# Optimization experiments

Hardware: AMD Instinct MI355X
Metric: run time of the kernel (lower is better)

## Reference

```python
import jax, jax.numpy as jnp
import numpy as np

D_MODEL = 512
D_FFN = 1024
B, N = 8, 2048


def setup_inputs() -> dict:
    key = jax.random.key(0)
    k1, k2, k3, k4, k5, k6 = jax.random.split(key, 6)
    x = jax.random.normal(k1, (B, N, D_MODEL), dtype=jnp.float32)
    interaction_mask = jax.random.randint(k2, (B, N, N), 0, 2).astype(jnp.float32)
    s1 = 1.0 / np.sqrt(D_MODEL)
    s2 = 1.0 / np.sqrt(D_FFN)
    W1 = jax.random.uniform(k3, (D_MODEL, D_FFN), jnp.float32, -s1, s1)
    b1 = jax.random.uniform(k4, (D_FFN,), jnp.float32, -s1, s1)
    W2 = jax.random.uniform(k5, (D_FFN, 3 * D_MODEL), jnp.float32, -s2, s2)
    b2 = jax.random.uniform(k6, (3 * D_MODEL,), jnp.float32, -s2, s2)
    return {"x": x, "interaction_mask": interaction_mask,
            "W1": W1, "b1": b1, "W2": W2, "b2": b2}


def reference(x, interaction_mask, W1, b1, W2, b2):
    # 2-layer FFN: Linear -> ReLU -> Linear (identity)
    h = jax.nn.relu(x @ W1 + b1)           # [B, N, d_ffn]
    kqv = h @ W2 + b2                        # [B, N, 3*d_model]
    k, q, v = jnp.split(kqv, 3, axis=-1)     # each [B, N, d_model]
    scale = D_MODEL ** -0.5
    # softmax-free scaled dot-product
    attn = jnp.einsum("bqd,bkd->bqk", q, k) * scale  # [B, N, N]
    attn = attn * interaction_mask
    return jnp.einsum("bqk,bkd->bqd", attn, v)        # [B, N, d_model]
```

## Files before the change

kernel.cpp:

```cpp
#include <hip/hip_runtime.h>
#include <hip/hip_bf16.h>

typedef __attribute__((ext_vector_type(8))) short bf16x8;
typedef __attribute__((ext_vector_type(4))) float f32x4;

#define NB 8
#define NN 2048
#define DM 512
#define DF 1024

__device__ __forceinline__ ushort f2b(float f) {
  union { __hip_bfloat16 h; ushort u; } c;
  c.h = __float2bfloat16(f);
  return c.u;
}
__device__ __forceinline__ float b2f(ushort u) {
  union { ushort u; __hip_bfloat16 h; } c;
  c.u = u;
  return __bfloat162float(c.h);
}

typedef __attribute__((address_space(1))) const void gvoid_t;
typedef __attribute__((address_space(3))) void svoid_t;
__device__ __forceinline__ void gload16(const void* g, void* s) {
  __builtin_amdgcn_global_load_lds((gvoid_t*)g, (svoid_t*)s, 16, 0, 0);
}

__device__ __forceinline__ void gemm_core_128(
    const ushort* __restrict__ A, const ushort* __restrict__ B,
    int K, int brow, int bcol, f32x4 (&acc)[4][4], ushort* smem)
{
  const int tid = threadIdx.x;
  const int w = tid >> 6, l = tid & 63;
  const int sr = (w << 3) + (l >> 3);
  const int sc = (((l & 7) ^ (l >> 3)) << 3);
  const int fr = l & 15;
  const int arow = ((w >> 1) << 6) + fr;
  const int brw  = ((w & 1) << 6) + fr;
  char* base = (char*)smem;
  char* A0 = base;          char* B0 = base + 16384;
  char* A1 = base + 32768;  char* B1 = base + 49152;

#pragma unroll
  for (int m = 0; m < 4; m++)
#pragma unroll
    for (int n = 0; n < 4; n++)
      acc[m][n] = (f32x4){0.f, 0.f, 0.f, 0.f};

  const ushort* Ap = A + (long)(brow + sr) * K + sc;
  const ushort* Bp = B + (long)(bcol + sr) * K + sc;
  const int nkt = K >> 6;

  auto stage = [&](char* Ad, char* Bd, int kt) {
#pragma unroll
    for (int i = 0; i < 4; i++) {
      gload16(Ap + (long)i * 32 * K + kt * 64, Ad + i * 4096 + (w << 10));
      gload16(Bp + (long)i * 32 * K + kt * 64, Bd + i * 4096 + (w << 10));
    }
  };
  auto compute = [&](const char* As_, const char* Bs_) {
#pragma unroll
    for (int kk = 0; kk < 2; kk++) {
      const int cx = ((((kk << 2) + (l >> 4)) ^ (l & 7)) << 4);
      bf16x8 a[4], b[4];
#pragma unroll
      for (int m = 0; m < 4; m++)
        a[m] = *(const bf16x8*)(As_ + (arow + m * 16) * 128 + cx);
#pragma unroll
      for (int n = 0; n < 4; n++)
        b[n] = *(const bf16x8*)(Bs_ + (brw + n * 16) * 128 + cx);
#pragma unroll
      for (int m = 0; m < 4; m++)
#pragma unroll
        for (int n = 0; n < 4; n++)
          acc[m][n] = __builtin_amdgcn_mfma_f32_16x16x32_bf16(a[m], b[n], acc[m][n], 0, 0, 0);
    }
  };

  stage(A0, B0, 0);
  __syncthreads();
  for (int kt = 0; kt < nkt; kt += 2) {
    stage(A1, B1, kt + 1);
    compute(A0, B0);
    __syncthreads();
    if (kt + 2 < nkt) stage(A0, B0, kt + 2);
    compute(A1, B1);
    __syncthreads();
  }
}

__device__ __forceinline__ void gemm_core_128_sb(
    const ushort* __restrict__ A, const ushort* __restrict__ B,
    int K, int brow, int bcol, f32x4 (&acc)[4][4], ushort* smem)
{
  ushort* As = smem;
  ushort* Bs = smem + 128 * 64;
  const int tid = threadIdx.x;
  const int w = tid >> 6, l = tid & 63;
  const int sr = (w << 3) + (l >> 3);
  const int sc = (((l & 7) ^ (l >> 3)) << 3);
  char* AsB = (char*)As;
  char* BsB = (char*)Bs;
  const int fr = l & 15;
  const int arow = ((w >> 1) << 6) + fr;
  const int brw  = ((w & 1) << 6) + fr;

#pragma unroll
  for (int m = 0; m < 4; m++)
#pragma unroll
    for (int n = 0; n < 4; n++)
      acc[m][n] = (f32x4){0.f, 0.f, 0.f, 0.f};

  const ushort* Ap = A + (long)(brow + sr) * K + sc;
  const ushort* Bp = B + (long)(bcol + sr) * K + sc;
  const int nkt = K >> 6;
  for (int kt = 0; kt < nkt; ++kt) {
#pragma unroll
    for (int i = 0; i < 4; i++) {
      gload16(Ap + (long)i * 32 * K, AsB + i * 4096 + (w << 10));
      gload16(Bp + (long)i * 32 * K, BsB + i * 4096 + (w << 10));
    }
    Ap += 64; Bp += 64;
    __syncthreads();
#pragma unroll
    for (int kk = 0; kk < 2; kk++) {
      const int cx = ((((kk << 2) + (l >> 4)) ^ (l & 7)) << 4);
      bf16x8 a[4], b[4];
#pragma unroll
      for (int m = 0; m < 4; m++)
        a[m] = *(const bf16x8*)(AsB + (arow + m * 16) * 128 + cx);
#pragma unroll
      for (int n = 0; n < 4; n++)
        b[n] = *(const bf16x8*)(BsB + (brw + n * 16) * 128 + cx);
#pragma unroll
      for (int m = 0; m < 4; m++)
#pragma unroll
        for (int n = 0; n < 4; n++)
          acc[m][n] = __builtin_amdgcn_mfma_f32_16x16x32_bf16(a[m], b[n], acc[m][n], 0, 0, 0);
    }
    __syncthreads();
  }
}

__device__ __forceinline__ void acc_to_lds_bf16(f32x4 (&acc)[4][4], ushort* smem) {
  const int tid = threadIdx.x, w = tid >> 6, l = tid & 63;
  const int r0l = ((w >> 1) << 6) + ((l >> 4) << 2);
  const int c0l = ((w & 1) << 6) + (l & 15);
#pragma unroll
  for (int n = 0; n < 4; n++)
#pragma unroll
    for (int m = 0; m < 4; m++)
#pragma unroll
      for (int j = 0; j < 4; j++)
        smem[(r0l + m * 16 + j) * 128 + (c0l + n * 16)] = f2b(acc[m][n][j]);
}


__global__ __launch_bounds__(256) void k_cvt(const float* __restrict__ in,
                                             ushort* __restrict__ out) {
  const long i = ((long)blockIdx.x * 256 + threadIdx.x) << 2;
  const float4 v = *(const float4*)(in + i);
  ushort4 o;
  o.x = f2b(v.x); o.y = f2b(v.y); o.z = f2b(v.z); o.w = f2b(v.w);
  *(ushort4*)(out + i) = o;
}

__device__ __forceinline__ float ld2f(const float* p, long i) { return p[i]; }
__device__ __forceinline__ float ld2f(const __hip_bfloat16* p, long i) { return __bfloat162float(p[i]); }

template <typename TIN>
__global__ __launch_bounds__(256) void k_tr(const TIN* __restrict__ in, ushort* __restrict__ out,
                                            int R, int C, long inB, long outB) {
  __shared__ float t[32][33];
  const long b = blockIdx.z;
  const TIN* ip = in + b * inB;
  ushort* op = out + b * outB;
  const int c0 = blockIdx.x << 5, r0 = blockIdx.y << 5;
  const int tx = threadIdx.x & 31, ty = threadIdx.x >> 5;
#pragma unroll
  for (int j = 0; j < 32; j += 8)
    t[ty + j][tx] = ld2f(ip, (long)(r0 + ty + j) * C + (c0 + tx));
  __syncthreads();
#pragma unroll
  for (int j = 0; j < 32; j += 8)
    op[(long)(c0 + ty + j) * R + (r0 + tx)] = f2b(t[tx][ty + j]);
}

__global__ __launch_bounds__(256) void k_gemm1(const ushort* __restrict__ xb,
                                               const ushort* __restrict__ w1t,
                                               const float* __restrict__ b1,
                                               ushort* __restrict__ hb) {
  __shared__ ushort smem[128 * 256];
  f32x4 acc[4][4];
  const int brow = blockIdx.x << 7, bcol = blockIdx.y << 7;
  gemm_core_128(xb, w1t, DM, brow, bcol, acc, smem);
  const int tid = threadIdx.x, w = tid >> 6, l = tid & 63;
  const int c0l = ((w & 1) << 6) + (l & 15);
#pragma unroll
  for (int n = 0; n < 4; n++) {
    const float bias = b1[bcol + c0l + n * 16];
#pragma unroll
    for (int m = 0; m < 4; m++)
#pragma unroll
      for (int j = 0; j < 4; j++) {
        float v = acc[m][n][j] + bias;
        acc[m][n][j] = v > 0.f ? v : 0.f;
      }
  }
  acc_to_lds_bf16(acc, smem);
  __syncthreads();
  const int rb = tid >> 4, cb = tid & 15;
#pragma unroll
  for (int i = 0; i < 8; i++) {
    const int row = i * 16 + rb;
    bf16x8 s = *(const bf16x8*)(smem + row * 128 + cb * 8);
    *(bf16x8*)(hb + (long)(brow + row) * DF + bcol + cb * 8) = s;
  }
}

__global__ __launch_bounds__(256) void k_gemm2(const ushort* __restrict__ hb,
                                               const ushort* __restrict__ w2t,
                                               const float* __restrict__ b2,
                                               ushort* __restrict__ kb,
                                               ushort* __restrict__ qb,
                                               ushort* __restrict__ vb) {
  __shared__ ushort smem[128 * 256];
  f32x4 acc[4][4];
  const int brow = blockIdx.x << 7, bcol = blockIdx.y << 7;
  gemm_core_128(hb, w2t, DF, brow, bcol, acc, smem);
  const int seg = bcol >> 9;
  ushort* dst = (seg == 0) ? kb : ((seg == 1) ? qb : vb);
  const float sc = (seg == 1) ? 0.04419417382415922f : 1.0f;
  const int tid = threadIdx.x, w = tid >> 6, l = tid & 63;
  const int c0l = ((w & 1) << 6) + (l & 15);
#pragma unroll
  for (int n = 0; n < 4; n++) {
    const float bias = b2[bcol + c0l + n * 16];
#pragma unroll
    for (int m = 0; m < 4; m++)
#pragma unroll
      for (int j = 0; j < 4; j++)
        acc[m][n][j] = (acc[m][n][j] + bias) * sc;
  }
  acc_to_lds_bf16(acc, smem);
  __syncthreads();
  const int rb = tid >> 4, cb = tid & 15;
  const int clb = bcol - (seg << 9);
#pragma unroll
  for (int i = 0; i < 8; i++) {
    const int row = i * 16 + rb;
    bf16x8 s = *(const bf16x8*)(smem + row * 128 + cb * 8);
    *(bf16x8*)(dst + (long)(brow + row) * DM + clb + cb * 8) = s;
  }
}

__global__ __launch_bounds__(256) void k_qk(const ushort* __restrict__ qb,
                                            const ushort* __restrict__ kb,
                                            const float* __restrict__ mask,
                                            ushort* __restrict__ Sbuf) {
  __shared__ ushort smem[128 * 128];
  const int orig = blockIdx.x;
  const int swz = (orig & 7) * 256 + (orig >> 3);
  const int bx = swz & 15, by = (swz >> 4) & 15, batch = swz >> 8;
  const int brow = bx << 7, bcol = by << 7;
  const ushort* A = qb + (long)batch * NN * DM;
  const ushort* Bm = kb + (long)batch * NN * DM;
  const float* mk = mask + (long)batch * NN * NN;
  ushort* S = Sbuf + (long)batch * NN * NN;

  f32x4 acc[4][4];
  gemm_core_128_sb(A, Bm, DM, brow, bcol, acc, smem);
  acc_to_lds_bf16(acc, smem);
  __syncthreads();

  const int tid = threadIdx.x, rb = tid >> 4, cb = tid & 15;
  float4 mreg[8][2];
#pragma unroll
  for (int i = 0; i < 8; i++) {
    const long goff = (long)(brow + i * 16 + rb) * NN + bcol + cb * 8;
    mreg[i][0] = *(const float4*)(mk + goff);
    mreg[i][1] = *(const float4*)(mk + goff + 4);
  }
#pragma unroll
  for (int i = 0; i < 8; i++) {
    const int row = i * 16 + rb;
    const long goff = (long)(brow + row) * NN + bcol + cb * 8;
    bf16x8 s = *(const bf16x8*)(smem + row * 128 + cb * 8);
    bf16x8 o;
    o[0] = (short)f2b(b2f((ushort)s[0]) * mreg[i][0].x);
    o[1] = (short)f2b(b2f((ushort)s[1]) * mreg[i][0].y);
    o[2] = (short)f2b(b2f((ushort)s[2]) * mreg[i][0].z);
    o[3] = (short)f2b(b2f((ushort)s[3]) * mreg[i][0].w);
    o[4] = (short)f2b(b2f((ushort)s[4]) * mreg[i][1].x);
    o[5] = (short)f2b(b2f((ushort)s[5]) * mreg[i][1].y);
    o[6] = (short)f2b(b2f((ushort)s[6]) * mreg[i][1].z);
    o[7] = (short)f2b(b2f((ushort)s[7]) * mreg[i][1].w);
    *(bf16x8*)(S + goff) = o;
  }
}

__global__ __launch_bounds__(256) void k_pv(const ushort* __restrict__ Sbuf,
                                            const ushort* __restrict__ vtb,
                                            float* __restrict__ out) {
  __shared__ ushort smem[128 * 256];
  const int batch = blockIdx.z;
  const ushort* A = Sbuf + (long)batch * NN * NN;
  const ushort* Bm = vtb + (long)batch * DM * NN;
  float* op = out + (long)batch * NN * DM;
  f32x4 acc[4][4];
  const int brow = blockIdx.x << 7, bcol = blockIdx.y << 7;
  gemm_core_128(A, Bm, NN, brow, bcol, acc, smem);
  const int tid = threadIdx.x, w = tid >> 6, l = tid & 63;
  const int r0 = brow + ((w >> 1) << 6) + ((l >> 4) << 2);
  const int c0 = bcol + ((w & 1) << 6) + (l & 15);
#pragma unroll
  for (int n = 0; n < 4; n++) {
    const int c = c0 + n * 16;
#pragma unroll
    for (int m = 0; m < 4; m++) {
      const int r = r0 + m * 16;
#pragma unroll
      for (int j = 0; j < 4; j++)
        op[(long)(r + j) * DM + c] = acc[m][n][j];
    }
  }
}

extern "C" void kernel_launch(void* const* d_in, const int* in_sizes, int n_in,
                              void* d_out, int out_size, void* d_ws, size_t ws_size,
                              hipStream_t stream) {
  const float* x    = (const float*)d_in[0];
  const float* mask = (const float*)d_in[1];
  const float* W1   = (const float*)d_in[2];
  const float* b1   = (const float*)d_in[3];
  const float* W2   = (const float*)d_in[4];
  const float* b2   = (const float*)d_in[5];
  float* out = (float*)d_out;

  char* ws = (char*)d_ws;
  size_t off = 0;
  auto alloc = [&](size_t n) { char* p = ws + off; off += (n + 255) & ~(size_t)255; return p; };
  ushort* xb  = (ushort*)alloc((size_t)NB * NN * DM * 2);
  ushort* hb  = (ushort*)alloc((size_t)NB * NN * DF * 2);
  ushort* w1t = (ushort*)alloc((size_t)DF * DM * 2);
  ushort* w2t = (ushort*)alloc((size_t)3 * DM * DF * 2);
  ushort* kb  = (ushort*)alloc((size_t)NB * NN * DM * 2);
  ushort* qb  = (ushort*)alloc((size_t)NB * NN * DM * 2);
  ushort* vb  = (ushort*)alloc((size_t)NB * NN * DM * 2);
  ushort* vtb = (ushort*)alloc((size_t)NB * NN * DM * 2);
  ushort* Sbuf = (ushort*)alloc((size_t)NB * NN * NN * 2);

  k_cvt<<<dim3(8192), dim3(256), 0, stream>>>(x, xb);
  k_tr<float><<<dim3(DF / 32, DM / 32, 1), dim3(256), 0, stream>>>(W1, w1t, DM, DF, 0, 0);
  k_tr<float><<<dim3(3 * DM / 32, DF / 32, 1), dim3(256), 0, stream>>>(W2, w2t, DF, 3 * DM, 0, 0);
  k_gemm1<<<dim3(NB * NN / 128, DF / 128), dim3(256), 0, stream>>>(xb, w1t, b1, hb);
  k_gemm2<<<dim3(NB * NN / 128, 3 * DM / 128), dim3(256), 0, stream>>>(hb, w2t, b2, kb, qb, vb);
  k_tr<__hip_bfloat16><<<dim3(DM / 32, NN / 32, NB), dim3(256), 0, stream>>>(
      (const __hip_bfloat16*)vb, vtb, NN, DM, (long)NN * DM, (long)DM * NN);
  k_qk<<<dim3(2048), dim3(256), 0, stream>>>(qb, kb, mask, Sbuf);
  k_pv<<<dim3(NN / 128, DM / 128, NB), dim3(256), 0, stream>>>(Sbuf, vtb, out);
}
```

Measured before the change: 220.0 us.

## Fuse V transpose into gemm2 epilogue, coalesce PV stores, simplify QK grid

New measurement: 209.7 us. 4.7% less time.

```diff
diff --git a/kernel.cpp b/kernel.cpp
--- a/kernel.cpp
+++ b/kernel.cpp
@@ -165,25 +165,18 @@
   *(ushort4*)(out + i) = o;
 }
 
-__device__ __forceinline__ float ld2f(const float* p, long i) { return p[i]; }
-__device__ __forceinline__ float ld2f(const __hip_bfloat16* p, long i) { return __bfloat162float(p[i]); }
-
-template <typename TIN>
-__global__ __launch_bounds__(256) void k_tr(const TIN* __restrict__ in, ushort* __restrict__ out,
-                                            int R, int C, long inB, long outB) {
+__global__ __launch_bounds__(256) void k_trw(const float* __restrict__ in, ushort* __restrict__ out,
+                                             int R, int C) {
   __shared__ float t[32][33];
-  const long b = blockIdx.z;
-  const TIN* ip = in + b * inB;
-  ushort* op = out + b * outB;
   const int c0 = blockIdx.x << 5, r0 = blockIdx.y << 5;
   const int tx = threadIdx.x & 31, ty = threadIdx.x >> 5;
 #pragma unroll
   for (int j = 0; j < 32; j += 8)
-    t[ty + j][tx] = ld2f(ip, (long)(r0 + ty + j) * C + (c0 + tx));
+    t[ty + j][tx] = in[(long)(r0 + ty + j) * C + (c0 + tx)];
   __syncthreads();
 #pragma unroll
   for (int j = 0; j < 32; j += 8)
-    op[(long)(c0 + ty + j) * R + (r0 + tx)] = f2b(t[tx][ty + j]);
+    out[(long)(c0 + ty + j) * R + (r0 + tx)] = f2b(t[tx][ty + j]);
 }
 
 __global__ __launch_bounds__(256) void k_gemm1(const ushort* __restrict__ xb,
@@ -223,13 +216,12 @@
                                                const float* __restrict__ b2,
                                                ushort* __restrict__ kb,
                                                ushort* __restrict__ qb,
-                                               ushort* __restrict__ vb) {
+                                               ushort* __restrict__ vtb) {
   __shared__ ushort smem[128 * 256];
   f32x4 acc[4][4];
   const int brow = blockIdx.x << 7, bcol = blockIdx.y << 7;
   gemm_core_128(hb, w2t, DF, brow, bcol, acc, smem);
   const int seg = bcol >> 9;
-  ushort* dst = (seg == 0) ? kb : ((seg == 1) ? qb : vb);
   const float sc = (seg == 1) ? 0.04419417382415922f : 1.0f;
   const int tid = threadIdx.x, w = tid >> 6, l = tid & 63;
   const int c0l = ((w & 1) << 6) + (l & 15);
@@ -244,13 +236,30 @@
   }
   acc_to_lds_bf16(acc, smem);
   __syncthreads();
-  const int rb = tid >> 4, cb = tid & 15;
   const int clb = bcol - (seg << 9);
-#pragma unroll
-  for (int i = 0; i < 8; i++) {
-    const int row = i * 16 + rb;
-    bf16x8 s = *(const bf16x8*)(smem + row * 128 + cb * 8);
-    *(bf16x8*)(dst + (long)(brow + row) * DM + clb + cb * 8) = s;
+  if (seg < 2) {
+    ushort* dst = (seg == 0) ? kb : qb;
+    const int rb = tid >> 4, cb = tid & 15;
+#pragma unroll
+    for (int i = 0; i < 8; i++) {
+      const int row = i * 16 + rb;
+      bf16x8 s = *(const bf16x8*)(smem + row * 128 + cb * 8);
+      *(bf16x8*)(dst + (long)(brow + row) * DM + clb + cb * 8) = s;
+    }
+  } else {
+    const int batch = brow >> 11;
+    const int rbase = brow & 2047;
+    const int c = tid & 127, rc = tid >> 7;
+    ushort* vt = vtb + (long)batch * DM * NN + (long)(clb + c) * NN + rbase;
+#pragma unroll
+    for (int it = 0; it < 8; ++it) {
+      const int chunk = rc * 8 + it;
+      bf16x8 o;
+#pragma unroll
+      for (int j = 0; j < 8; ++j)
+        o[j] = (short)smem[(chunk * 8 + j) * 128 + c];
+      *(bf16x8*)(vt + chunk * 8) = o;
+    }
   }
 }
 
@@ -259,42 +268,33 @@
                                             const float* __restrict__ mask,
                                             ushort* __restrict__ Sbuf) {
   __shared__ ushort smem[128 * 128];
-  const int orig = blockIdx.x;
-  const int swz = (orig & 7) * 256 + (orig >> 3);
-  const int bx = swz & 15, by = (swz >> 4) & 15, batch = swz >> 8;
-  const int brow = bx << 7, bcol = by << 7;
+  const int batch = blockIdx.z;
   const ushort* A = qb + (long)batch * NN * DM;
   const ushort* Bm = kb + (long)batch * NN * DM;
   const float* mk = mask + (long)batch * NN * NN;
   ushort* S = Sbuf + (long)batch * NN * NN;
-
   f32x4 acc[4][4];
+  const int brow = blockIdx.x << 7, bcol = blockIdx.y << 7;
   gemm_core_128_sb(A, Bm, DM, brow, bcol, acc, smem);
   acc_to_lds_bf16(acc, smem);
   __syncthreads();
-
   const int tid = threadIdx.x, rb = tid >> 4, cb = tid & 15;
-  float4 mreg[8][2];
-#pragma unroll
-  for (int i = 0; i < 8; i++) {
-    const long goff = (long)(brow + i * 16 + rb) * NN + bcol + cb * 8;
-    mreg[i][0] = *(const float4*)(mk + goff);
-    mreg[i][1] = *(const float4*)(mk + goff + 4);
-  }
 #pragma unroll
   for (int i = 0; i < 8; i++) {
     const int row = i * 16 + rb;
     const long goff = (long)(brow + row) * NN + bcol + cb * 8;
     bf16x8 s = *(const bf16x8*)(smem + row * 128 + cb * 8);
+    const float4 m0 = *(const float4*)(mk + goff);
+    const float4 m1 = *(const float4*)(mk + goff + 4);
     bf16x8 o;
-    o[0] = (short)f2b(b2f((ushort)s[0]) * mreg[i][0].x);
-    o[1] = (short)f2b(b2f((ushort)s[1]) * mreg[i][0].y);
-    o[2] = (short)f2b(b2f((ushort)s[2]) * mreg[i][0].z);
-    o[3] = (short)f2b(b2f((ushort)s[3]) * mreg[i][0].w);
-    o[4] = (short)f2b(b2f((ushort)s[4]) * mreg[i][1].x);
-    o[5] = (short)f2b(b2f((ushort)s[5]) * mreg[i][1].y);
-    o[6] = (short)f2b(b2f((ushort)s[6]) * mreg[i][1].z);
-    o[7] = (short)f2b(b2f((ushort)s[7]) * mreg[i][1].w);
+    o[0] = (short)f2b(b2f((ushort)s[0]) * m0.x);
+    o[1] = (short)f2b(b2f((ushort)s[1]) * m0.y);
+    o[2] = (short)f2b(b2f((ushort)s[2]) * m0.z);
+    o[3] = (short)f2b(b2f((ushort)s[3]) * m0.w);
+    o[4] = (short)f2b(b2f((ushort)s[4]) * m1.x);
+    o[5] = (short)f2b(b2f((ushort)s[5]) * m1.y);
+    o[6] = (short)f2b(b2f((ushort)s[6]) * m1.z);
+    o[7] = (short)f2b(b2f((ushort)s[7]) * m1.w);
     *(bf16x8*)(S + goff) = o;
   }
 }
@@ -310,19 +310,24 @@
   f32x4 acc[4][4];
   const int brow = blockIdx.x << 7, bcol = blockIdx.y << 7;
   gemm_core_128(A, Bm, NN, brow, bcol, acc, smem);
+  float* fs = (float*)smem;
   const int tid = threadIdx.x, w = tid >> 6, l = tid & 63;
-  const int r0 = brow + ((w >> 1) << 6) + ((l >> 4) << 2);
-  const int c0 = bcol + ((w & 1) << 6) + (l & 15);
-#pragma unroll
-  for (int n = 0; n < 4; n++) {
-    const int c = c0 + n * 16;
-#pragma unroll
-    for (int m = 0; m < 4; m++) {
-      const int r = r0 + m * 16;
+  const int r0l = ((w >> 1) << 6) + ((l >> 4) << 2);
+  const int c0l = ((w & 1) << 6) + (l & 15);
+#pragma unroll
+  for (int n = 0; n < 4; n++)
+#pragma unroll
+    for (int m = 0; m < 4; m++)
 #pragma unroll
       for (int j = 0; j < 4; j++)
-        op[(long)(r + j) * DM + c] = acc[m][n][j];
-    }
+        fs[(r0l + m * 16 + j) * 128 + (c0l + n * 16)] = acc[m][n][j];
+  __syncthreads();
+  const int rg = tid >> 5, l32 = tid & 31;
+#pragma unroll
+  for (int p = 0; p < 16; ++p) {
+    const int row = p * 8 + rg;
+    const float4 v = *(const float4*)(fs + row * 128 + l32 * 4);
+    *(float4*)(op + (long)(brow + row) * DM + bcol + l32 * 4) = v;
   }
 }
 
@@ -346,17 +351,14 @@
   ushort* w2t = (ushort*)alloc((size_t)3 * DM * DF * 2);
   ushort* kb  = (ushort*)alloc((size_t)NB * NN * DM * 2);
   ushort* qb  = (ushort*)alloc((size_t)NB * NN * DM * 2);
-  ushort* vb  = (ushort*)alloc((size_t)NB * NN * DM * 2);
   ushort* vtb = (ushort*)alloc((size_t)NB * NN * DM * 2);
   ushort* Sbuf = (ushort*)alloc((size_t)NB * NN * NN * 2);
 
   k_cvt<<<dim3(8192), dim3(256), 0, stream>>>(x, xb);
-  k_tr<float><<<dim3(DF / 32, DM / 32, 1), dim3(256), 0, stream>>>(W1, w1t, DM, DF, 0, 0);
-  k_tr<float><<<dim3(3 * DM / 32, DF / 32, 1), dim3(256), 0, stream>>>(W2, w2t, DF, 3 * DM, 0, 0);
+  k_trw<<<dim3(DF / 32, DM / 32), dim3(256), 0, stream>>>(W1, w1t, DM, DF);
+  k_trw<<<dim3(3 * DM / 32, DF / 32), dim3(256), 0, stream>>>(W2, w2t, DF, 3 * DM);
   k_gemm1<<<dim3(NB * NN / 128, DF / 128), dim3(256), 0, stream>>>(xb, w1t, b1, hb);
-  k_gemm2<<<dim3(NB * NN / 128, 3 * DM / 128), dim3(256), 0, stream>>>(hb, w2t, b2, kb, qb, vb);
-  k_tr<__hip_bfloat16><<<dim3(DM / 32, NN / 32, NB), dim3(256), 0, stream>>>(
-      (const __hip_bfloat16*)vb, vtb, NN, DM, (long)NN * DM, (long)DM * NN);
-  k_qk<<<dim3(2048), dim3(256), 0, stream>>>(qb, kb, mask, Sbuf);
+  k_gemm2<<<dim3(NB * NN / 128, 3 * DM / 128), dim3(256), 0, stream>>>(hb, w2t, b2, kb, qb, vtb);
+  k_qk<<<dim3(NN / 128, NN / 128, NB), dim3(256), 0, stream>>>(qb, kb, mask, Sbuf);
   k_pv<<<dim3(NN / 128, DM / 128, NB), dim3(256), 0, stream>>>(Sbuf, vtb, out);
 }
```
